# Performance work log

Measured on AMD Instinct MI355X. Metric: run time of the kernel, lower is better.

Reference implementation:

```python
import jax, jax.numpy as jnp
import numpy as np
import math

H = 1024   # d_model
NH = 32    # N // 2 state size
L_LEN = 4096
DT_MIN, DT_MAX = 0.001, 0.1


def setup_inputs() -> dict:
    key = jax.random.key(0)
    k1, k2, k3, k4 = jax.random.split(key, 4)
    C = jax.random.normal(k1, (H, NH, 2), dtype=jnp.float32)  # view_as_real complex C
    log_dt = (jax.random.uniform(k2, (H,), dtype=jnp.float32)
              * (math.log(DT_MAX) - math.log(DT_MIN)) + math.log(DT_MIN))
    # log of positive real parts (original: log(|Re(eig)|) repeated over H)
    log_A_real = jnp.log(0.5 + jax.random.uniform(k3, (H, NH), dtype=jnp.float32) * NH)
    A_imag = jax.random.normal(k4, (H, NH), dtype=jnp.float32) * math.pi
    return {"C": C, "log_dt": log_dt, "log_A_real": log_A_real,
            "A_imag": A_imag, "L": L_LEN}


def reference(C, log_dt, log_A_real, A_imag, L):
    dt = jnp.exp(log_dt)                                  # [H]
    Cc = C[..., 0] + 1j * C[..., 1]                       # [H, N] complex64
    A = -jnp.exp(log_A_real) - 1j * A_imag                # [H, N]
    dtA = A * dt[:, None]                                 # [H, N]
    # Vandermonde: exp(dtA)^l for l in [0, L)
    K = dtA[:, :, None] * jnp.arange(L, dtype=jnp.float32)  # [H, N, L]
    Cc = Cc * (jnp.exp(dtA) - 1.0) / A                    # [H, N]
    K = 2.0 * jnp.einsum('hn,hnl->hl', Cc, jnp.exp(K)).real  # [H, L]
    return K
```

## Files before the change

kernel.cpp:

```cpp
#include <hip/hip_runtime.h>
#include <math.h>


#define HH 1024
#define NH 32
#define LL 4096
#define BLOCK 256
#define SPLIT 4
#define STRIDE 1024

#define TWO_PI 6.28318530717958647692f
#define INV_TWO_PI 0.15915494309189533577f

__device__ __forceinline__ float sin_rev(float r) {
    float d;
    asm("v_sin_f32 %0, %1" : "=v"(d) : "v"(r));
    return d;
}
__device__ __forceinline__ float cos_rev(float r) {
    float d;
    asm("v_cos_f32 %0, %1" : "=v"(d) : "v"(r));
    return d;
}

__global__ __launch_bounds__(BLOCK) void s4_vandermonde(
    const float* __restrict__ C,
    const float* __restrict__ log_dt,
    const float* __restrict__ log_A_real,
    const float* __restrict__ A_imag,
    float* __restrict__ out)
{
    __shared__ float2 sW16[NH][16];
    __shared__ float2 sW1[NH][16];
    __shared__ float4 sP[NH];
    __shared__ float4 sAux[NH];

    const int h = blockIdx.x >> 2;
    const int s = blockIdx.x & 3;
    const int t = threadIdx.x;

    if (t < NH) {
        const int n = t;
        const float dt  = __expf(log_dt[h]);
        const float Are = -__expf(log_A_real[h * NH + n]);
        const float Aim = -A_imag[h * NH + n];
        const float re = Are * dt;
        const float im = Aim * dt;
        float s1, c1;
        __sincosf(im, &s1, &c1);
        const float er1 = __expf(re);
        const float X = er1 * c1 - 1.0f;
        const float Y = er1 * s1;
        const float C0 = C[(h * NH + n) * 2 + 0];
        const float C1 = C[(h * NH + n) * 2 + 1];
        const float nr = C0 * X - C1 * Y;
        const float ni = C0 * Y + C1 * X;
        const float inv = 2.0f / (Are * Are + Aim * Aim);
        const float ctr = (nr * Are + ni * Aim) * inv;
        const float cti = (ni * Are - nr * Aim) * inv;
        const float fm = im * INV_TWO_PI;

        const float erS = __expf(re * 1024.0f);
        double revd = (double)im * (double)INV_TWO_PI * 1024.0;
        revd -= floor(revd);
        float sS, cS;
        __sincosf((float)revd * TWO_PI, &sS, &cS);

        sP[n]   = make_float4(re, erS * cS, erS * sS, erS * erS);
        sAux[n] = make_float4(fm, ctr, cti, re);
    }
    __syncthreads();

    {
        const int n = t >> 3;
        const int j = t & 7;
        const float4 aux = sAux[n];
        const float fm = aux.x, ctr = aux.y, cti = aux.z, re = aux.w;
#pragma unroll
        for (int q = 0; q < 2; ++q) {
            const int e = j + q * 8;
            {
                const float er = __expf(re * (float)e);
                float rev = fm * (float)e;
                rev -= floorf(rev);
                sW1[n][e] = make_float2(er * cos_rev(rev), er * sin_rev(rev));
            }
            {
                const float m = (float)(s * 256 + 16 * e);
                const float er = __expf(re * m);
                float rev = fm * m;
                rev -= floorf(rev);
                const float br = er * cos_rev(rev);
                const float bi = er * sin_rev(rev);
                sW16[n][e] = make_float2(ctr * br - cti * bi,
                                         ctr * bi + cti * br);
            }
        }
    }
    __syncthreads();

    float acc0 = 0.0f, acc1 = 0.0f, acc2 = 0.0f, acc3 = 0.0f;
    const float lf = (float)(s * BLOCK + t);
    const int hi = t >> 4, lo = t & 15;

    for (int n = 0; n < NH; ++n) {
        const float4 P = sP[n];
        if (P.x * lf < -16.0f) continue;
        const float2 a2 = sW16[n][hi];
        const float2 b2 = sW1[n][lo];
        const float vr = a2.x * b2.x - a2.y * b2.y;
        const float vi = a2.x * b2.y + a2.y * b2.x;
        acc0 += vr;
        const float u1 = vr * P.y - vi * P.z;
        acc1 += u1;
        const float aS = P.y + P.y;
        const float u2 = aS * u1 - P.w * vr;
        acc2 += u2;
        const float u3 = aS * u2 - P.w * u1;
        acc3 += u3;
    }

    float* o = out + h * LL + s * BLOCK + t;
    o[0]          = acc0;
    o[STRIDE]     = acc1;
    o[2 * STRIDE] = acc2;
    o[3 * STRIDE] = acc3;
}

extern "C" void kernel_launch(void* const* d_in, const int* in_sizes, int n_in,
                              void* d_out, int out_size, void* d_ws, size_t ws_size,
                              hipStream_t stream) {
    const float* C          = (const float*)d_in[0];
    const float* log_dt     = (const float*)d_in[1];
    const float* log_A_real = (const float*)d_in[2];
    const float* A_imag     = (const float*)d_in[3];
    float* out              = (float*)d_out;

    s4_vandermonde<<<dim3(HH * SPLIT), dim3(BLOCK), 0, stream>>>(
        C, log_dt, log_A_real, A_imag, out);
}
```

Measured before the change: 83.52 us.

## Process one row per block with eight-step Chebyshev recurrence over 512-wide chunks

```diff
diff --git a/kernel.cpp b/kernel.cpp
--- a/kernel.cpp
+++ b/kernel.cpp
@@ -5,9 +5,9 @@
 #define HH 1024
 #define NH 32
 #define LL 4096
-#define BLOCK 256
-#define SPLIT 4
-#define STRIDE 1024
+#define BLOCK 512
+#define KCH 8
+#define STRIDE 512
 
 #define TWO_PI 6.28318530717958647692f
 #define INV_TWO_PI 0.15915494309189533577f
@@ -30,13 +30,12 @@
     const float* __restrict__ A_imag,
     float* __restrict__ out)
 {
-    __shared__ float2 sW16[NH][16];
+    __shared__ float2 sW16[NH][32];
     __shared__ float2 sW1[NH][16];
     __shared__ float4 sP[NH];
     __shared__ float4 sAux[NH];
 
-    const int h = blockIdx.x >> 2;
-    const int s = blockIdx.x & 3;
+    const int h = blockIdx.x;
     const int t = threadIdx.x;
 
     if (t < NH) {
@@ -60,8 +59,8 @@
         const float cti = (ni * Are - nr * Aim) * inv;
         const float fm = im * INV_TWO_PI;
 
-        const float erS = __expf(re * 1024.0f);
-        double revd = (double)im * (double)INV_TWO_PI * 1024.0;
+        const float erS = __expf(re * 512.0f);
+        double revd = (double)fm * 512.0;
         revd -= floor(revd);
         float sS, cS;
         __sincosf((float)revd * TWO_PI, &sS, &cS);
@@ -71,60 +70,62 @@
     }
     __syncthreads();
 
-    {
-        const int n = t >> 3;
-        const int j = t & 7;
+#pragma unroll
+    for (int q = 0; q < 3; ++q) {
+        const int idx = t + q * BLOCK;
+        const int n = idx / 48;
+        const int j = idx - n * 48;
         const float4 aux = sAux[n];
         const float fm = aux.x, ctr = aux.y, cti = aux.z, re = aux.w;
-#pragma unroll
-        for (int q = 0; q < 2; ++q) {
-            const int e = j + q * 8;
-            {
-                const float er = __expf(re * (float)e);
-                float rev = fm * (float)e;
-                rev -= floorf(rev);
-                sW1[n][e] = make_float2(er * cos_rev(rev), er * sin_rev(rev));
-            }
-            {
-                const float m = (float)(s * 256 + 16 * e);
-                const float er = __expf(re * m);
-                float rev = fm * m;
-                rev -= floorf(rev);
-                const float br = er * cos_rev(rev);
-                const float bi = er * sin_rev(rev);
-                sW16[n][e] = make_float2(ctr * br - cti * bi,
-                                         ctr * bi + cti * br);
-            }
+        if (j < 16) {
+            const float m = (float)j;
+            const float er = __expf(re * m);
+            float rev = fm * m;
+            rev -= floorf(rev);
+            sW1[n][j] = make_float2(er * cos_rev(rev), er * sin_rev(rev));
+        } else {
+            const int a = j - 16;
+            const float m = (float)(a * 16);
+            const float er = __expf(re * m);
+            float rev = fm * m;
+            rev -= floorf(rev);
+            const float br = er * cos_rev(rev);
+            const float bi = er * sin_rev(rev);
+            sW16[n][a] = make_float2(ctr * br - cti * bi, ctr * bi + cti * br);
         }
     }
     __syncthreads();
 
-    float acc0 = 0.0f, acc1 = 0.0f, acc2 = 0.0f, acc3 = 0.0f;
-    const float lf = (float)(s * BLOCK + t);
+    float acc[KCH];
+#pragma unroll
+    for (int k = 0; k < KCH; ++k) acc[k] = 0.0f;
+
+    const float wminf = (float)(t & ~63);
     const int hi = t >> 4, lo = t & 15;
 
     for (int n = 0; n < NH; ++n) {
         const float4 P = sP[n];
-        if (P.x * lf < -16.0f) continue;
+        if (P.x * wminf < -16.0f) continue;
         const float2 a2 = sW16[n][hi];
         const float2 b2 = sW1[n][lo];
         const float vr = a2.x * b2.x - a2.y * b2.y;
         const float vi = a2.x * b2.y + a2.y * b2.x;
-        acc0 += vr;
-        const float u1 = vr * P.y - vi * P.z;
-        acc1 += u1;
+        float u0 = vr;
+        float u1 = vr * P.y - vi * P.z;
+        acc[0] += u0;
+        acc[1] += u1;
         const float aS = P.y + P.y;
-        const float u2 = aS * u1 - P.w * vr;
-        acc2 += u2;
-        const float u3 = aS * u2 - P.w * u1;
-        acc3 += u3;
+#pragma unroll
+        for (int k = 2; k < KCH; ++k) {
+            const float u2 = aS * u1 - P.w * u0;
+            acc[k] += u2;
+            u0 = u1; u1 = u2;
+        }
     }
 
-    float* o = out + h * LL + s * BLOCK + t;
-    o[0]          = acc0;
-    o[STRIDE]     = acc1;
-    o[2 * STRIDE] = acc2;
-    o[3 * STRIDE] = acc3;
+    float* o = out + h * LL + t;
+#pragma unroll
+    for (int k = 0; k < KCH; ++k) o[k * STRIDE] = acc[k];
 }
 
 extern "C" void kernel_launch(void* const* d_in, const int* in_sizes, int n_in,
@@ -136,6 +137,6 @@
     const float* A_imag     = (const float*)d_in[3];
     float* out              = (float*)d_out;
 
-    s4_vandermonde<<<dim3(HH * SPLIT), dim3(BLOCK), 0, stream>>>(
+    s4_vandermonde<<<dim3(HH), dim3(BLOCK), 0, stream>>>(
         C, log_dt, log_A_real, A_imag, out);
 }
```

Measured after the change: 84.75 us. Within noise of the previous version (+1.5%).
